# Optimization experiments

Hardware: AMD Instinct MI355X
Metric: run time of the kernel (lower is better)

## Reference

```python
import jax, jax.numpy as jnp
from jax import lax
import numpy as np

B, T, V, H = 512, 512, 96, 128


def setup_inputs() -> dict:
    key = jax.random.key(0)
    ks = jax.random.split(key, 8)
    # one-hot character inputs [B, T, V]
    idx = jax.random.randint(ks[0], (B, T), 0, V)
    x = jax.nn.one_hot(idx, V, dtype=jnp.float32)
    s_ih = 1.0 / np.sqrt(H)  # PyTorch nn.RNN init: U(-1/sqrt(H), 1/sqrt(H))
    W_ih = jax.random.uniform(ks[1], (H, V), jnp.float32, -s_ih, s_ih)
    b_ih = jax.random.uniform(ks[2], (H,), jnp.float32, -s_ih, s_ih)
    W_hh = jax.random.uniform(ks[3], (H, H), jnp.float32, -s_ih, s_ih)
    b_hh = jax.random.uniform(ks[4], (H,), jnp.float32, -s_ih, s_ih)
    s_fc = 1.0 / np.sqrt(H)
    W_fc = jax.random.uniform(ks[5], (V, H), jnp.float32, -s_fc, s_fc)
    b_fc = jax.random.uniform(ks[6], (V,), jnp.float32, -s_fc, s_fc)
    return {"x": x, "W_ih": W_ih, "b_ih": b_ih, "W_hh": W_hh,
            "b_hh": b_hh, "W_fc": W_fc, "b_fc": b_fc}


def reference(x, W_ih, b_ih, W_hh, b_hh, W_fc, b_fc):
    # Precompute input projection for all timesteps (batched GEMM):
    # for one-hot x this is effectively an embedding row gather.
    xW = jnp.einsum('btv,hv->bth', x, W_ih) + b_ih  # [B, T, H]

    def step(h, xt):  # h: [B, H], xt: [B, H]
        h_new = jnp.tanh(xt + h @ W_hh.T + b_hh)
        return h_new, None

    h0 = jnp.zeros((x.shape[0], W_hh.shape[0]), x.dtype)
    hT, _ = lax.scan(step, h0, jnp.swapaxes(xW, 0, 1))  # scan over T
    # fc on the last hidden state only
    return hT @ W_fc.T + b_fc  # [B, V]
```

## Files before the change

kernel.cpp:

```cpp
#include <hip/hip_runtime.h>

#define B_ 512
#define T_ 512
#define V_ 96
#define H_ 128
#define K2F 2.8853900817779268f

typedef _Float16 half8 __attribute__((ext_vector_type(8)));
typedef float    f32x4 __attribute__((ext_vector_type(4)));

__global__ __launch_bounds__(256) void onehot_idx_kernel(
    const float4* __restrict__ x4, int n4, int* __restrict__ idx)
{
    int stride = gridDim.x * blockDim.x;
    for (int e4 = blockIdx.x * blockDim.x + threadIdx.x; e4 < n4; e4 += stride) {
        float4 v = x4[e4];
        int base = e4 * 4;
        if (v.x > 0.5f) idx[(base + 0) / V_] = (base + 0) % V_;
        if (v.y > 0.5f) idx[(base + 1) / V_] = (base + 1) % V_;
        if (v.z > 0.5f) idx[(base + 2) / V_] = (base + 2) % V_;
        if (v.w > 0.5f) idx[(base + 3) / V_] = (base + 3) % V_;
    }
}

__global__ __launch_bounds__(256) void build_xwg_kernel(
    const float* __restrict__ W_ih, const float* __restrict__ b_ih,
    const float* __restrict__ b_hh, float* __restrict__ xwg)
{
    int e = blockIdx.x * 256 + threadIdx.x;
    if (e < V_ * H_) {
        int v = e >> 7, up = e & 127;
        int u = (up & 7) * 16 + (up >> 3);
        xwg[e] = (W_ih[u * V_ + v] + b_ih[u] + b_hh[u]) * K2F;
    }
}

__global__ __launch_bounds__(256) void build_wB_kernel(
    const float* __restrict__ W_hh, _Float16* __restrict__ wB)
{
    int e = blockIdx.x * 256 + threadIdx.x;
    if (e < 16384) {
        int reg = e & 7, lane = (e >> 3) & 63, nt = (e >> 9) & 7, ks = e >> 12;
        int unit = ks * 32 + (lane >> 4) * 8 + reg;
        int n    = nt * 16 + (lane & 15);
        wB[e] = (_Float16)(K2F * W_hh[n * H_ + unit]);
    }
}

__global__ __launch_bounds__(256) void build_wBfc_kernel(
    const float* __restrict__ W_fc, _Float16* __restrict__ wBfc)
{
    int e = blockIdx.x * 256 + threadIdx.x;
    if (e < 12288) {
        int reg = e & 7, lane = (e >> 3) & 63;
        int nt = (e >> 9) % 6, ks = e / 3072;
        int unit = ks * 32 + (lane >> 4) * 8 + reg;
        int n    = nt * 16 + (lane & 15);
        wBfc[e] = (_Float16)W_fc[n * H_ + unit];
    }
}

__global__ __launch_bounds__(256, 1) void rnn_mfma4_kernel(
    const uint4* __restrict__ wBg, const uint4* __restrict__ wBfcg,
    const float* __restrict__ xwg, const int* __restrict__ idx,
    const float* __restrict__ b_fc, float* __restrict__ out)
{
    const int bb  = blockIdx.x;
    const int tid = threadIdx.x;
    const int w   = tid >> 6;
    const int l   = tid & 63;
    const int lo  = l & 15, g = l >> 4;

    __shared__ _Float16      hs[2][16][136];
    __shared__ unsigned char idxT[(T_ + 2) * 16];

    for (int e = tid; e < 16 * T_; e += 256) {
        int row = e >> 9, t = e & 511;
        idxT[t * 16 + row] = (unsigned char)idx[(bb * 16 + row) * T_ + t];
    }
    if (tid < 32) idxT[T_ * 16 + tid] = 0;
    for (int e = tid; e < 16 * 136; e += 256)
        hs[0][e / 136][e % 136] = (_Float16)0.f;

    uint4 wb[4][2];
    #pragma unroll
    for (int ks = 0; ks < 4; ++ks)
        #pragma unroll
        for (int q = 0; q < 2; ++q)
            wb[ks][q] = wBg[(ks * 8 + 2 * w + q) * 64 + l];

    float2 xwc[4];
    unsigned idw;
    __builtin_memcpy(&idw, &idxT[0 * 16 + 4 * g], 4);
    #pragma unroll
    for (int j = 0; j < 4; ++j) {
        int id = (idw >> (8 * j)) & 255;
        xwc[j] = *(const float2*)(xwg + id * 128 + lo * 8 + 2 * w);
    }
    __builtin_memcpy(&idw, &idxT[1 * 16 + 4 * g], 4);

    __syncthreads();

    int cur = 0;
    #pragma clang loop unroll(disable)
    for (int t = 0; t < T_; ++t) {
        half8 aF[4];
        #pragma unroll
        for (int ks = 0; ks < 4; ++ks)
            __builtin_memcpy(&aF[ks], &hs[cur][lo][ks * 32 + g * 8], 16);

        float2 xwn[4];
        #pragma unroll
        for (int j = 0; j < 4; ++j) {
            int id = (idw >> (8 * j)) & 255;
            xwn[j] = *(const float2*)(xwg + id * 128 + lo * 8 + 2 * w);
        }
        __builtin_memcpy(&idw, &idxT[(t + 2) * 16 + 4 * g], 4);

        f32x4 acc0 = {0.f, 0.f, 0.f, 0.f}, acc1 = {0.f, 0.f, 0.f, 0.f};
        #pragma unroll
        for (int ks = 0; ks < 4; ++ks) {
            union { uint4 u; half8 h; } u0, u1;
            u0.u = wb[ks][0]; u1.u = wb[ks][1];
            acc0 = __builtin_amdgcn_mfma_f32_16x16x32_f16(aF[ks], u0.h, acc0, 0, 0, 0);
            acc1 = __builtin_amdgcn_mfma_f32_16x16x32_f16(aF[ks], u1.h, acc1, 0, 0, 0);
        }
        #pragma unroll
        for (int j = 0; j < 4; ++j) {
            float E0 = __builtin_amdgcn_exp2f(acc0[j] + xwc[j].x);
            float E1 = __builtin_amdgcn_exp2f(acc1[j] + xwc[j].y);
            float h0 = 1.0f - 2.0f * __builtin_amdgcn_rcpf(E0 + 1.0f);
            float h1 = 1.0f - 2.0f * __builtin_amdgcn_rcpf(E1 + 1.0f);
            hs[cur ^ 1][4 * g + j][(2 * w + 0) * 16 + lo] = (_Float16)h0;
            hs[cur ^ 1][4 * g + j][(2 * w + 1) * 16 + lo] = (_Float16)h1;
        }
        #pragma unroll
        for (int j = 0; j < 4; ++j) xwc[j] = xwn[j];
        cur ^= 1;
        __syncthreads();
    }

    half8 aE[4];
    #pragma unroll
    for (int ks = 0; ks < 4; ++ks)
        __builtin_memcpy(&aE[ks], &hs[cur][lo][ks * 32 + g * 8], 16);
    #pragma unroll
    for (int q = 0; q < 2; ++q) {
        const int NT = 2 * w + q;
        if (NT < 6) {
            float bf = b_fc[NT * 16 + lo];
            f32x4 acc = {bf, bf, bf, bf};
            #pragma unroll
            for (int ks = 0; ks < 4; ++ks) {
                union { uint4 u; half8 h; } ub;
                ub.u = wBfcg[(ks * 6 + NT) * 64 + l];
                acc = __builtin_amdgcn_mfma_f32_16x16x32_f16(aE[ks], ub.h, acc, 0, 0, 0);
            }
            #pragma unroll
            for (int j = 0; j < 4; ++j)
                out[(bb * 16 + 4 * g + j) * V_ + NT * 16 + lo] = acc[j];
        }
    }
}

extern "C" void kernel_launch(void* const* d_in, const int* in_sizes, int n_in,
                              void* d_out, int out_size, void* d_ws, size_t ws_size,
                              hipStream_t stream)
{
    const float* x    = (const float*)d_in[0];
    const float* W_ih = (const float*)d_in[1];
    const float* b_ih = (const float*)d_in[2];
    const float* W_hh = (const float*)d_in[3];
    const float* b_hh = (const float*)d_in[4];
    const float* W_fc = (const float*)d_in[5];
    const float* b_fc = (const float*)d_in[6];
    float* out = (float*)d_out;

    char* ws = (char*)d_ws;
    int*      idx  = (int*)ws;
    float*    xwg  = (float*)(ws + (size_t)B_ * T_ * 4);
    _Float16* wB   = (_Float16*)((char*)xwg + V_ * H_ * 4);
    _Float16* wBfc = (_Float16*)((char*)wB + 16384 * 2);

    const int n4 = (B_ * T_ * V_) / 4;
    hipLaunchKernelGGL(onehot_idx_kernel, dim3(2048), dim3(256), 0, stream,
                       (const float4*)x, n4, idx);
    hipLaunchKernelGGL(build_xwg_kernel, dim3((V_ * H_ + 255) / 256), dim3(256),
                       0, stream, W_ih, b_ih, b_hh, xwg);
    hipLaunchKernelGGL(build_wB_kernel, dim3(64), dim3(256), 0, stream, W_hh, wB);
    hipLaunchKernelGGL(build_wBfc_kernel, dim3(48), dim3(256), 0, stream, W_fc, wBfc);
    hipLaunchKernelGGL(rnn_mfma4_kernel, dim3(B_ / 16), dim3(256), 0, stream,
                       (const uint4*)wB, (const uint4*)wBfc, xwg, idx, b_fc, out);
}
```

Baseline: 233.0 us.

## Pack two independent 16-row batch groups per 512-thread block and split MFMA accumulators

Each block now runs two independent 16-row batch groups of the recurrence. Each group has four waves and its own hidden-state and index buffers in shared memory, which halves the grid from 32 to 16 blocks. The k-loop of MFMAs is also split into two independent accumulator chains that are summed afterwards, shortening the dependent MFMA chain on the serial critical path. The cost is that both groups now share one __syncthreads per step, and the grid uses fewer CUs.

```diff
diff --git a/kernel.cpp b/kernel.cpp
--- a/kernel.cpp
+++ b/kernel.cpp
@@ -60,7 +60,7 @@
     }
 }
 
-__global__ __launch_bounds__(256, 1) void rnn_mfma4_kernel(
+__global__ __launch_bounds__(512, 1) void rnn_mfma8_kernel(
     const uint4* __restrict__ wBg, const uint4* __restrict__ wBfcg,
     const float* __restrict__ xwg, const int* __restrict__ idx,
     const float* __restrict__ b_fc, float* __restrict__ out)
@@ -68,36 +68,42 @@
     const int bb  = blockIdx.x;
     const int tid = threadIdx.x;
     const int w   = tid >> 6;
+    const int grp = w >> 2;
+    const int ww  = w & 3;
     const int l   = tid & 63;
     const int lo  = l & 15, g = l >> 4;
-
-    __shared__ _Float16      hs[2][16][136];
-    __shared__ unsigned char idxT[(T_ + 2) * 16];
-
-    for (int e = tid; e < 16 * T_; e += 256) {
+    const int rowbase = bb * 32 + grp * 16;
+
+    __shared__ _Float16      hs[2][2][16][136];
+    __shared__ unsigned char idxT[2][(T_ + 2) * 16];
+
+    for (int e = tid; e < 32 * T_; e += 512) {
         int row = e >> 9, t = e & 511;
-        idxT[t * 16 + row] = (unsigned char)idx[(bb * 16 + row) * T_ + t];
-    }
-    if (tid < 32) idxT[T_ * 16 + tid] = 0;
-    for (int e = tid; e < 16 * 136; e += 256)
-        hs[0][e / 136][e % 136] = (_Float16)0.f;
+        idxT[row >> 4][t * 16 + (row & 15)] =
+            (unsigned char)idx[(bb * 32 + row) * T_ + t];
+    }
+    if (tid < 64) idxT[tid >> 5][T_ * 16 + (tid & 31)] = 0;
+    for (int e = tid; e < 2 * 16 * 136; e += 512) {
+        int gz = e / 2176, rem = e % 2176;
+        hs[gz][0][rem / 136][rem % 136] = (_Float16)0.f;
+    }
 
     uint4 wb[4][2];
     #pragma unroll
     for (int ks = 0; ks < 4; ++ks)
         #pragma unroll
         for (int q = 0; q < 2; ++q)
-            wb[ks][q] = wBg[(ks * 8 + 2 * w + q) * 64 + l];
+            wb[ks][q] = wBg[(ks * 8 + 2 * ww + q) * 64 + l];
 
     float2 xwc[4];
     unsigned idw;
-    __builtin_memcpy(&idw, &idxT[0 * 16 + 4 * g], 4);
+    __builtin_memcpy(&idw, &idxT[grp][0 * 16 + 4 * g], 4);
     #pragma unroll
     for (int j = 0; j < 4; ++j) {
         int id = (idw >> (8 * j)) & 255;
-        xwc[j] = *(const float2*)(xwg + id * 128 + lo * 8 + 2 * w);
-    }
-    __builtin_memcpy(&idw, &idxT[1 * 16 + 4 * g], 4);
+        xwc[j] = *(const float2*)(xwg + id * 128 + lo * 8 + 2 * ww);
+    }
+    __builtin_memcpy(&idw, &idxT[grp][1 * 16 + 4 * g], 4);
 
     __syncthreads();
 
@@ -107,32 +113,38 @@
         half8 aF[4];
         #pragma unroll
         for (int ks = 0; ks < 4; ++ks)
-            __builtin_memcpy(&aF[ks], &hs[cur][lo][ks * 32 + g * 8], 16);
+            __builtin_memcpy(&aF[ks], &hs[grp][cur][lo][ks * 32 + g * 8], 16);
 
         float2 xwn[4];
         #pragma unroll
         for (int j = 0; j < 4; ++j) {
             int id = (idw >> (8 * j)) & 255;
-            xwn[j] = *(const float2*)(xwg + id * 128 + lo * 8 + 2 * w);
-        }
-        __builtin_memcpy(&idw, &idxT[(t + 2) * 16 + 4 * g], 4);
-
-        f32x4 acc0 = {0.f, 0.f, 0.f, 0.f}, acc1 = {0.f, 0.f, 0.f, 0.f};
-        #pragma unroll
-        for (int ks = 0; ks < 4; ++ks) {
-            union { uint4 u; half8 h; } u0, u1;
-            u0.u = wb[ks][0]; u1.u = wb[ks][1];
-            acc0 = __builtin_amdgcn_mfma_f32_16x16x32_f16(aF[ks], u0.h, acc0, 0, 0, 0);
-            acc1 = __builtin_amdgcn_mfma_f32_16x16x32_f16(aF[ks], u1.h, acc1, 0, 0, 0);
-        }
+            xwn[j] = *(const float2*)(xwg + id * 128 + lo * 8 + 2 * ww);
+        }
+        __builtin_memcpy(&idw, &idxT[grp][(t + 2) * 16 + 4 * g], 4);
+
+        f32x4 p0 = {0.f,0.f,0.f,0.f}, p1 = {0.f,0.f,0.f,0.f};
+        f32x4 q0 = {0.f,0.f,0.f,0.f}, q1 = {0.f,0.f,0.f,0.f};
+        #pragma unroll
+        for (int ks = 0; ks < 2; ++ks) {
+            union { uint4 u; half8 h; } u0, u1, u2, u3;
+            u0.u = wb[ks][0];     u1.u = wb[ks][1];
+            u2.u = wb[ks + 2][0]; u3.u = wb[ks + 2][1];
+            p0 = __builtin_amdgcn_mfma_f32_16x16x32_f16(aF[ks],     u0.h, p0, 0, 0, 0);
+            p1 = __builtin_amdgcn_mfma_f32_16x16x32_f16(aF[ks],     u1.h, p1, 0, 0, 0);
+            q0 = __builtin_amdgcn_mfma_f32_16x16x32_f16(aF[ks + 2], u2.h, q0, 0, 0, 0);
+            q1 = __builtin_amdgcn_mfma_f32_16x16x32_f16(aF[ks + 2], u3.h, q1, 0, 0, 0);
+        }
+        f32x4 acc0 = p0 + q0, acc1 = p1 + q1;
+
         #pragma unroll
         for (int j = 0; j < 4; ++j) {
             float E0 = __builtin_amdgcn_exp2f(acc0[j] + xwc[j].x);
             float E1 = __builtin_amdgcn_exp2f(acc1[j] + xwc[j].y);
             float h0 = 1.0f - 2.0f * __builtin_amdgcn_rcpf(E0 + 1.0f);
             float h1 = 1.0f - 2.0f * __builtin_amdgcn_rcpf(E1 + 1.0f);
-            hs[cur ^ 1][4 * g + j][(2 * w + 0) * 16 + lo] = (_Float16)h0;
-            hs[cur ^ 1][4 * g + j][(2 * w + 1) * 16 + lo] = (_Float16)h1;
+            hs[grp][cur ^ 1][4 * g + j][(2 * ww + 0) * 16 + lo] = (_Float16)h0;
+            hs[grp][cur ^ 1][4 * g + j][(2 * ww + 1) * 16 + lo] = (_Float16)h1;
         }
         #pragma unroll
         for (int j = 0; j < 4; ++j) xwc[j] = xwn[j];
@@ -143,10 +155,10 @@
     half8 aE[4];
     #pragma unroll
     for (int ks = 0; ks < 4; ++ks)
-        __builtin_memcpy(&aE[ks], &hs[cur][lo][ks * 32 + g * 8], 16);
+        __builtin_memcpy(&aE[ks], &hs[grp][cur][lo][ks * 32 + g * 8], 16);
     #pragma unroll
     for (int q = 0; q < 2; ++q) {
-        const int NT = 2 * w + q;
+        const int NT = 2 * ww + q;
         if (NT < 6) {
             float bf = b_fc[NT * 16 + lo];
             f32x4 acc = {bf, bf, bf, bf};
@@ -158,7 +170,7 @@
             }
             #pragma unroll
             for (int j = 0; j < 4; ++j)
-                out[(bb * 16 + 4 * g + j) * V_ + NT * 16 + lo] = acc[j];
+                out[(rowbase + 4 * g + j) * V_ + NT * 16 + lo] = acc[j];
         }
     }
 }
@@ -189,6 +201,6 @@
                        0, stream, W_ih, b_ih, b_hh, xwg);
     hipLaunchKernelGGL(build_wB_kernel, dim3(64), dim3(256), 0, stream, W_hh, wB);
     hipLaunchKernelGGL(build_wBfc_kernel, dim3(48), dim3(256), 0, stream, W_fc, wBfc);
-    hipLaunchKernelGGL(rnn_mfma4_kernel, dim3(B_ / 16), dim3(256), 0, stream,
+    hipLaunchKernelGGL(rnn_mfma8_kernel, dim3(B_ / 32), dim3(512), 0, stream,
                        (const uint4*)wB, (const uint4*)wBfc, xwg, idx, b_fc, out);
 }
```

Result: slower. 320.1 us (+37.4%).

## Stage input-projection table in LDS and split MFMA accumulation chains

Applied to the files above, without the earlier changes.

The 96x128 precomputed input-projection table is copied into shared memory, padded to a stride of 132, once per block. Each timestep then gathers its xW rows from LDS instead of global memory, which also removes the two-step software prefetch of indices and rows. The MFMA K-reduction is split into two independent accumulator chains that are summed at the end, which shortens the dependent MFMA latency chain on the serial recurrence path. This costs about 48KB of extra LDS per block and puts LDS gather latency directly on the critical path instead of hiding it behind prefetch.

```diff
diff --git a/kernel.cpp b/kernel.cpp
--- a/kernel.cpp
+++ b/kernel.cpp
@@ -4,6 +4,7 @@
 #define T_ 512
 #define V_ 96
 #define H_ 128
+#define XST 132
 #define K2F 2.8853900817779268f
 
 typedef _Float16 half8 __attribute__((ext_vector_type(8)));
@@ -71,14 +72,18 @@
     const int l   = tid & 63;
     const int lo  = l & 15, g = l >> 4;
 
+    __shared__ float         xwl[V_ * XST];
     __shared__ _Float16      hs[2][16][136];
-    __shared__ unsigned char idxT[(T_ + 2) * 16];
+    __shared__ unsigned char idxT[T_ * 16];
 
+    for (int e = tid; e < V_ * H_; e += 256) {
+        int v = e >> 7, up = e & 127;
+        xwl[v * XST + up] = xwg[e];
+    }
     for (int e = tid; e < 16 * T_; e += 256) {
         int row = e >> 9, t = e & 511;
         idxT[t * 16 + row] = (unsigned char)idx[(bb * 16 + row) * T_ + t];
     }
-    if (tid < 32) idxT[T_ * 16 + tid] = 0;
     for (int e = tid; e < 16 * 136; e += 256)
         hs[0][e / 136][e % 136] = (_Float16)0.f;
 
@@ -89,42 +94,40 @@
         for (int q = 0; q < 2; ++q)
             wb[ks][q] = wBg[(ks * 8 + 2 * w + q) * 64 + l];
 
-    float2 xwc[4];
-    unsigned idw;
-    __builtin_memcpy(&idw, &idxT[0 * 16 + 4 * g], 4);
-    #pragma unroll
-    for (int j = 0; j < 4; ++j) {
-        int id = (idw >> (8 * j)) & 255;
-        xwc[j] = *(const float2*)(xwg + id * 128 + lo * 8 + 2 * w);
-    }
-    __builtin_memcpy(&idw, &idxT[1 * 16 + 4 * g], 4);
-
     __syncthreads();
 
     int cur = 0;
     #pragma clang loop unroll(disable)
     for (int t = 0; t < T_; ++t) {
+        unsigned idw;
+        __builtin_memcpy(&idw, &idxT[t * 16 + 4 * g], 4);
+
         half8 aF[4];
         #pragma unroll
         for (int ks = 0; ks < 4; ++ks)
             __builtin_memcpy(&aF[ks], &hs[cur][lo][ks * 32 + g * 8], 16);
 
-        float2 xwn[4];
+        float2 xwc[4];
         #pragma unroll
         for (int j = 0; j < 4; ++j) {
             int id = (idw >> (8 * j)) & 255;
-            xwn[j] = *(const float2*)(xwg + id * 128 + lo * 8 + 2 * w);
+            __builtin_memcpy(&xwc[j], &xwl[id * XST + lo * 8 + 2 * w], 8);
         }
-        __builtin_memcpy(&idw, &idxT[(t + 2) * 16 + 4 * g], 4);
 
-        f32x4 acc0 = {0.f, 0.f, 0.f, 0.f}, acc1 = {0.f, 0.f, 0.f, 0.f};
+        f32x4 p0 = {0.f,0.f,0.f,0.f}, p1 = {0.f,0.f,0.f,0.f};
+        f32x4 q0 = {0.f,0.f,0.f,0.f}, q1 = {0.f,0.f,0.f,0.f};
         #pragma unroll
-        for (int ks = 0; ks < 4; ++ks) {
-            union { uint4 u; half8 h; } u0, u1;
-            u0.u = wb[ks][0]; u1.u = wb[ks][1];
-            acc0 = __builtin_amdgcn_mfma_f32_16x16x32_f16(aF[ks], u0.h, acc0, 0, 0, 0);
-            acc1 = __builtin_amdgcn_mfma_f32_16x16x32_f16(aF[ks], u1.h, acc1, 0, 0, 0);
+        for (int ks = 0; ks < 2; ++ks) {
+            union { uint4 u; half8 h; } u0, u1, u2, u3;
+            u0.u = wb[ks][0];     u1.u = wb[ks][1];
+            u2.u = wb[ks + 2][0]; u3.u = wb[ks + 2][1];
+            p0 = __builtin_amdgcn_mfma_f32_16x16x32_f16(aF[ks],     u0.h, p0, 0, 0, 0);
+            p1 = __builtin_amdgcn_mfma_f32_16x16x32_f16(aF[ks],     u1.h, p1, 0, 0, 0);
+            q0 = __builtin_amdgcn_mfma_f32_16x16x32_f16(aF[ks + 2], u2.h, q0, 0, 0, 0);
+            q1 = __builtin_amdgcn_mfma_f32_16x16x32_f16(aF[ks + 2], u3.h, q1, 0, 0, 0);
         }
+        f32x4 acc0 = p0 + q0, acc1 = p1 + q1;
+
         #pragma unroll
         for (int j = 0; j < 4; ++j) {
             float E0 = __builtin_amdgcn_exp2f(acc0[j] + xwc[j].x);
@@ -134,8 +137,6 @@
             hs[cur ^ 1][4 * g + j][(2 * w + 0) * 16 + lo] = (_Float16)h0;
             hs[cur ^ 1][4 * g + j][(2 * w + 1) * 16 + lo] = (_Float16)h1;
         }
-        #pragma unroll
-        for (int j = 0; j < 4; ++j) xwc[j] = xwn[j];
         cur ^= 1;
         __syncthreads();
     }
```

Result: faster. 224.9 us (-3.5%).
